# Optimization experiments

Hardware: AMD Instinct MI355X
Metric: run time of the kernel (lower is better)

Reference implementation:

```python
import jax, jax.numpy as jnp
import numpy as np
from jax import lax


def _box_conv3d(x, win):
    k = jnp.ones((1, 1, win, win, win), x.dtype) / float(win ** 3)
    pad = win // 2
    return lax.conv_general_dilated(
        x, k,
        window_strides=(1, 1, 1),
        padding=[(pad, pad)] * 3,
        dimension_numbers=('NCDHW', 'OIDHW', 'NCDHW'),
    )


def setup_inputs() -> dict:
    key = jax.random.key(0)
    k1, k2 = jax.random.split(key)
    shape = (1, 1, 160, 192, 224)
    pred = jax.random.uniform(k1, shape, dtype=jnp.float32)
    target = jax.random.uniform(k2, shape, dtype=jnp.float32)
    return {'pred': pred, 'target': target, 'window_size': 9}


def reference(pred, target, window_size):
    Ii = target
    Ji = pred
    win = window_size
    mu1 = _box_conv3d(Ii, win)
    mu2 = _box_conv3d(Ji, win)
    mu1_sq = mu1 * mu1
    mu2_sq = mu2 * mu2
    mu1_mu2 = mu1 * mu2
    sigma1_sq = _box_conv3d(Ii * Ii, win) - mu1_sq
    sigma2_sq = _box_conv3d(Ji * Ji, win) - mu2_sq
    sigma12 = _box_conv3d(Ii * Ji, win) - mu1_mu2
    eps = jnp.finfo(sigma12.dtype).eps
    cc = sigma12 * sigma12 / jnp.maximum(sigma1_sq * sigma2_sq, eps)
    return -jnp.mean(cc)
```

## Files before the change

### kernel.cpp

```cpp
#include <hip/hip_runtime.h>
#include <hip/hip_fp16.h>

#define D_  160
#define H_  192
#define W_  224
#define HW_ (H_ * W_)
#define HW2_ (HW_ / 2)
#define N_  (D_ * H_ * W_)
#define INV729 (1.0f / 729.0f)
#define HSEG 12
#define NSEG (H_ / HSEG)
#define NROW (HSEG + 9)
#define UPD  (NSEG * 2)


__device__ __forceinline__ unsigned pack2(float a, float b) {
    const __half2 h = __floats2half2_rn(a, b);
    return *(const unsigned*)&h;
}

__global__ __launch_bounds__(256) void k_passWH(const float* __restrict__ pred,
                                                const float* __restrict__ targ,
                                                uint4* __restrict__ outA,
                                                unsigned* __restrict__ outB,
                                                double* __restrict__ acc) {
    __shared__ __attribute__((aligned(16))) float lds[4][2][2][128];
    if (blockIdx.x == 0 && threadIdx.x == 0) *acc = 0.0;

    const int wid  = threadIdx.x >> 6;
    const int lane = threadIdx.x & 63;
    const int unit = blockIdx.x * 4 + wid;
    const int d    = unit / UPD;
    const int rem  = unit % UPD;
    const int half = rem & 1;
    const int h0   = (rem >> 1) * HSEG;
    const long dbase = (long)d * HW_;
    const int wbase = half * 112;

    const bool isld = (lane < 60);
    const int  arr  = (lane >= 30) ? 1 : 0;
    const int  jj   = arr ? lane - 30 : lane;
    const int  ws   = wbase - 4 + 4 * jj;
    const bool geom = isld && (ws >= 0) && (ws + 3 < W_);
    const int  wsc  = ws < 0 ? 0 : (ws > W_ - 4 ? W_ - 4 : ws);
    const float* gsrc = (arr ? pred : targ) + dbase + wsc;

    float2 q[5][9];
    #pragma unroll
    for (int c = 0; c < 5; ++c)
        #pragma unroll
        for (int k = 0; k < 9; ++k) q[c][k] = make_float2(0.f, 0.f);
    float S0[5] = {0,0,0,0,0}, S1[5] = {0,0,0,0,0};

    auto fetch = [&](int p) -> float4 {
        const int hh = h0 - 5 + p;
        const int hc = hh < 0 ? 0 : (hh >= H_ ? H_ - 1 : hh);
        float4 f = *(const float4*)(gsrc + (long)hc * W_);
        if (!(geom && hh >= 0 && hh < H_)) f = make_float4(0.f, 0.f, 0.f, 0.f);
        return f;
    };

    float4 pf[4];
    pf[0] = fetch(0); pf[1] = fetch(1); pf[2] = fetch(2); pf[3] = fetch(3);
    if (isld) *(float4*)&lds[wid][0][arr][4 * jj] = pf[0];
    pf[0] = fetch(4);

    #pragma unroll
    for (int p = 0; p < NROW; ++p) {
        if (isld) *(float4*)&lds[wid][(p + 1) & 1][arr][4 * jj] = pf[(p + 1) & 3];
        pf[(p + 1) & 3] = fetch(p + 5);

        if (lane < 56) {
            float a[10], b[10];
            #pragma unroll
            for (int m = 0; m < 5; ++m) {
                const float2 va = *(const float2*)&lds[wid][p & 1][0][2 * lane + 2 * m];
                const float2 vb = *(const float2*)&lds[wid][p & 1][1][2 * lane + 2 * m];
                a[2*m] = va.x; a[2*m+1] = va.y;
                b[2*m] = vb.x; b[2*m+1] = vb.y;
            }
            float sI = 0.f, sJ = 0.f, sII = 0.f, sJJ = 0.f, sIJ = 0.f;
            #pragma unroll
            for (int kk = 0; kk < 9; ++kk) {
                sI  += a[kk];          sJ  += b[kk];
                sII += a[kk] * a[kk];  sJJ += b[kk] * b[kk];
                sIJ += a[kk] * b[kk];
            }
            float w0[5], w1[5];
            w0[0] = sI;  w1[0] = sI  + a[9] - a[0];
            w0[1] = sJ;  w1[1] = sJ  + b[9] - b[0];
            w0[2] = sII; w1[2] = sII + a[9]*a[9] - a[0]*a[0];
            w0[3] = sJJ; w1[3] = sJJ + b[9]*b[9] - b[0]*b[0];
            w0[4] = sIJ; w1[4] = sIJ + a[9]*b[9] - a[0]*b[0];

            const int ph = p % 9;
            #pragma unroll
            for (int c = 0; c < 5; ++c) {
                S0[c] += w0[c] - q[c][ph].x;
                S1[c] += w1[c] - q[c][ph].y;
                q[c][ph].x = w0[c];
                q[c][ph].y = w1[c];
            }
            if (p >= 9) {
                const long rb = dbase + (long)(h0 + p - 9) * W_;
                uint4 oA;
                oA.x = pack2(S0[0], S0[1]); oA.y = pack2(S0[2], S0[3]);
                oA.z = pack2(S1[0], S1[1]); oA.w = pack2(S1[2], S1[3]);
                outA[rb / 2 + half * 56 + lane] = oA;
                outB[rb / 2 + half * 56 + lane] = pack2(S0[4], S1[4]);
            }
        }
    }
}

__global__ __launch_bounds__(256) void k_passD(const uint4* __restrict__ bufA,
                                               const unsigned* __restrict__ bufB,
                                               double* __restrict__ acc) {
    const int DSEG = D_ / 8;
    const int p2 = blockIdx.x * blockDim.x + threadIdx.x;
    const int d0 = blockIdx.y * DSEG;

    float2 q[5][9], S[5];
    #pragma unroll
    for (int c = 0; c < 5; ++c) S[c] = make_float2(0.f, 0.f);

    #pragma unroll
    for (int k = 0; k < 9; ++k) {
        const int dd = d0 - 5 + k;
        uint4 va = make_uint4(0u, 0u, 0u, 0u);
        unsigned vb = 0u;
        if (dd >= 0) {
            va = bufA[(long)dd * HW2_ + p2];
            vb = bufB[(long)dd * HW2_ + p2];
        }
        const float2 a01 = __half22float2(*(const __half2*)&va.x);
        const float2 a23 = __half22float2(*(const __half2*)&va.y);
        const float2 b01 = __half22float2(*(const __half2*)&va.z);
        const float2 b23 = __half22float2(*(const __half2*)&va.w);
        const float2 c44 = __half22float2(*(const __half2*)&vb);
        q[0][k] = make_float2(a01.x, b01.x); S[0].x += a01.x; S[0].y += b01.x;
        q[1][k] = make_float2(a01.y, b01.y); S[1].x += a01.y; S[1].y += b01.y;
        q[2][k] = make_float2(a23.x, b23.x); S[2].x += a23.x; S[2].y += b23.x;
        q[3][k] = make_float2(a23.y, b23.y); S[3].x += a23.y; S[3].y += b23.y;
        q[4][k] = make_float2(c44.x, c44.y); S[4].x += c44.x; S[4].y += c44.y;
    }

    float myacc = 0.f;
    #pragma unroll
    for (int j = 0; j < DSEG; ++j) {
        const int dd = d0 + 4 + j;
        uint4 va = make_uint4(0u, 0u, 0u, 0u);
        unsigned vb = 0u;
        if (dd < D_) {
            va = bufA[(long)dd * HW2_ + p2];
            vb = bufB[(long)dd * HW2_ + p2];
        }
        const float2 a01 = __half22float2(*(const __half2*)&va.x);
        const float2 a23 = __half22float2(*(const __half2*)&va.y);
        const float2 b01 = __half22float2(*(const __half2*)&va.z);
        const float2 b23 = __half22float2(*(const __half2*)&va.w);
        const float2 c44 = __half22float2(*(const __half2*)&vb);
        const float2 nv[5] = {
            make_float2(a01.x, b01.x), make_float2(a01.y, b01.y),
            make_float2(a23.x, b23.x), make_float2(a23.y, b23.y),
            make_float2(c44.x, c44.y)
        };
        const int ph = j % 9;
        #pragma unroll
        for (int c = 0; c < 5; ++c) {
            S[c].x += nv[c].x - q[c][ph].x;
            S[c].y += nv[c].y - q[c][ph].y;
            q[c][ph] = nv[c];
        }
        #pragma unroll
        for (int e = 0; e < 2; ++e) {
            const float mu1 = (e ? S[0].y : S[0].x) * INV729;
            const float mu2 = (e ? S[1].y : S[1].x) * INV729;
            const float s1  = (e ? S[2].y : S[2].x) * INV729 - mu1 * mu1;
            const float s2  = (e ? S[3].y : S[3].x) * INV729 - mu2 * mu2;
            const float s12 = (e ? S[4].y : S[4].x) * INV729 - mu1 * mu2;
            const float den = fmaxf(s1 * s2, 1.1920929e-7f);
            myacc += (s12 * s12) / den;
        }
    }

    __shared__ float red[256];
    red[threadIdx.x] = myacc;
    __syncthreads();
    #pragma unroll
    for (int s = 128; s > 0; s >>= 1) {
        if (threadIdx.x < s) red[threadIdx.x] += red[threadIdx.x + s];
        __syncthreads();
    }
    if (threadIdx.x == 0) atomicAdd(acc, (double)red[0]);
}

__global__ void k_fin(const double* __restrict__ acc, float* __restrict__ out) {
    out[0] = (float)(-(*acc) / (double)N_);
}

extern "C" void kernel_launch(void* const* d_in, const int* in_sizes, int n_in,
                              void* d_out, int out_size, void* d_ws, size_t ws_size,
                              hipStream_t stream) {
    const float* pred = (const float*)d_in[0];
    const float* targ = (const float*)d_in[1];

    uint4*    bufA = (uint4*)d_ws;
    unsigned* bufB = (unsigned*)((char*)d_ws + (size_t)(N_ / 2) * 16);
    double*   acc  = (double*)((char*)d_ws + (size_t)(N_ / 2) * 16 + (size_t)(N_ / 2) * 4);
    float*    out  = (float*)d_out;

    k_passWH<<<D_ * UPD / 4, 256, 0, stream>>>(pred, targ, bufA, bufB, acc);
    dim3 g3(HW2_ / 256, 8);
    k_passD<<<g3, 256, 0, stream>>>(bufA, bufB, acc);
    k_fin<<<1, 1, 0, stream>>>(acc, out);
}
```

Measured before the change: 56.49 us.

## Stream WH-pass rows straight into LDS with async global_load_lds ring buffer

Replaces the register prefetch plus explicit LDS store in the W/H pass with direct global-to-LDS loads into an 8-slot per-wave ring, waiting on hand-tuned vmcnt counts. Out-of-range rows and chunks read from a small zeroed page, so the masking moves off the load path. The aim is to cut VGPR pressure and the LDS write instructions while keeping about six rows in flight. Accumulator zeroing moves into a separate init kernel, which adds one launch. The vmcnt values depend on how many loads the compiler emits and their order, so any change in code generation could break correctness or stall.

Measured after the change: 65.67 us. +16.3%, slower.

```diff
diff --git a/kernel.cpp b/kernel.cpp
--- a/kernel.cpp
+++ b/kernel.cpp
@@ -12,21 +12,38 @@
 #define NSEG (H_ / HSEG)
 #define NROW (HSEG + 9)
 #define UPD  (NSEG * 2)
-
+#define RING 8
+
+
+typedef __attribute__((address_space(1))) const unsigned GU;
+typedef __attribute__((address_space(3))) unsigned LU;
 
 __device__ __forceinline__ unsigned pack2(float a, float b) {
     const __half2 h = __floats2half2_rn(a, b);
     return *(const unsigned*)&h;
+}
+
+__device__ __forceinline__ void vmwait_step(int p) {
+    if (p <= 9)       asm volatile("s_waitcnt vmcnt(2)"  ::: "memory");
+    else if (p == 10) asm volatile("s_waitcnt vmcnt(4)"  ::: "memory");
+    else if (p == 11) asm volatile("s_waitcnt vmcnt(6)"  ::: "memory");
+    else if (p == 12) asm volatile("s_waitcnt vmcnt(8)"  ::: "memory");
+    else if (p == 13) asm volatile("s_waitcnt vmcnt(10)" ::: "memory");
+    else              asm volatile("s_waitcnt vmcnt(12)" ::: "memory");
+    __builtin_amdgcn_sched_barrier(0);
+}
+
+__global__ void k_init(double* acc, float* zpage) {
+    if (threadIdx.x == 0) *acc = 0.0;
+    if (threadIdx.x < 16) zpage[threadIdx.x] = 0.f;
 }
 
 __global__ __launch_bounds__(256) void k_passWH(const float* __restrict__ pred,
                                                 const float* __restrict__ targ,
                                                 uint4* __restrict__ outA,
                                                 unsigned* __restrict__ outB,
-                                                double* __restrict__ acc) {
-    __shared__ __attribute__((aligned(16))) float lds[4][2][2][128];
-    if (blockIdx.x == 0 && threadIdx.x == 0) *acc = 0.0;
-
+                                                const float* __restrict__ zpage) {
+    __shared__ __attribute__((aligned(16))) float lds[4][RING][256];
     const int wid  = threadIdx.x >> 6;
     const int lane = threadIdx.x & 63;
     const int unit = blockIdx.x * 4 + wid;
@@ -37,13 +54,10 @@
     const long dbase = (long)d * HW_;
     const int wbase = half * 112;
 
-    const bool isld = (lane < 60);
-    const int  arr  = (lane >= 30) ? 1 : 0;
-    const int  jj   = arr ? lane - 30 : lane;
-    const int  ws   = wbase - 4 + 4 * jj;
-    const bool geom = isld && (ws >= 0) && (ws + 3 < W_);
-    const int  wsc  = ws < 0 ? 0 : (ws > W_ - 4 ? W_ - 4 : ws);
-    const float* gsrc = (arr ? pred : targ) + dbase + wsc;
+    const int  jj  = (lane < 30) ? lane : lane - 30;
+    const int  ws  = wbase - 4 + 4 * jj;
+    const bool chunk_ok = (lane < 60) && (ws >= 0) && (ws + 3 < W_);
+    const float* csrc = ((lane < 30) ? targ : pred) + dbase + ws;
 
     float2 q[5][9];
     #pragma unroll
@@ -52,30 +66,26 @@
         for (int k = 0; k < 9; ++k) q[c][k] = make_float2(0.f, 0.f);
     float S0[5] = {0,0,0,0,0}, S1[5] = {0,0,0,0,0};
 
-    auto fetch = [&](int p) -> float4 {
-        const int hh = h0 - 5 + p;
-        const int hc = hh < 0 ? 0 : (hh >= H_ ? H_ - 1 : hh);
-        float4 f = *(const float4*)(gsrc + (long)hc * W_);
-        if (!(geom && hh >= 0 && hh < H_)) f = make_float4(0.f, 0.f, 0.f, 0.f);
-        return f;
+    auto issue = [&](int r) {
+        const int hh = h0 - 5 + r;
+        const bool rok = (hh >= 0) && (hh < H_);
+        const float* ga = (chunk_ok && rok) ? (csrc + (long)hh * W_) : zpage;
+        __builtin_amdgcn_global_load_lds((GU*)ga, (LU*)&lds[wid][r & 7][0], 16, 0, 0);
     };
 
-    float4 pf[4];
-    pf[0] = fetch(0); pf[1] = fetch(1); pf[2] = fetch(2); pf[3] = fetch(3);
-    if (isld) *(float4*)&lds[wid][0][arr][4 * jj] = pf[0];
-    pf[0] = fetch(4);
+    issue(0); issue(1); issue(2); issue(3); issue(4); issue(5);
 
     #pragma unroll
     for (int p = 0; p < NROW; ++p) {
-        if (isld) *(float4*)&lds[wid][(p + 1) & 1][arr][4 * jj] = pf[(p + 1) & 3];
-        pf[(p + 1) & 3] = fetch(p + 5);
+        vmwait_step(p);
 
         if (lane < 56) {
+            const float* buf = &lds[wid][p & 7][0];
             float a[10], b[10];
             #pragma unroll
             for (int m = 0; m < 5; ++m) {
-                const float2 va = *(const float2*)&lds[wid][p & 1][0][2 * lane + 2 * m];
-                const float2 vb = *(const float2*)&lds[wid][p & 1][1][2 * lane + 2 * m];
+                const float2 va = *(const float2*)&buf[2 * lane + 2 * m];
+                const float2 vb = *(const float2*)&buf[120 + 2 * lane + 2 * m];
                 a[2*m] = va.x; a[2*m+1] = va.y;
                 b[2*m] = vb.x; b[2*m+1] = vb.y;
             }
@@ -110,6 +120,8 @@
                 outB[rb / 2 + half * 56 + lane] = pack2(S0[4], S1[4]);
             }
         }
+        issue(p + 6);
+        __builtin_amdgcn_sched_barrier(0);
     }
 }
 
@@ -205,12 +217,19 @@
     const float* pred = (const float*)d_in[0];
     const float* targ = (const float*)d_in[1];
 
-    uint4*    bufA = (uint4*)d_ws;
-    unsigned* bufB = (unsigned*)((char*)d_ws + (size_t)(N_ / 2) * 16);
-    double*   acc  = (double*)((char*)d_ws + (size_t)(N_ / 2) * 16 + (size_t)(N_ / 2) * 4);
-    float*    out  = (float*)d_out;
-
-    k_passWH<<<D_ * UPD / 4, 256, 0, stream>>>(pred, targ, bufA, bufB, acc);
+    const size_t offA = 0;
+    const size_t offB = (size_t)(N_ / 2) * 16;
+    const size_t offAcc = offB + (size_t)(N_ / 2) * 4;
+    const size_t offZ = offAcc + 64;
+
+    uint4*    bufA  = (uint4*)((char*)d_ws + offA);
+    unsigned* bufB  = (unsigned*)((char*)d_ws + offB);
+    double*   acc   = (double*)((char*)d_ws + offAcc);
+    float*    zpage = (float*)((char*)d_ws + offZ);
+    float*    out   = (float*)d_out;
+
+    k_init<<<1, 64, 0, stream>>>(acc, zpage);
+    k_passWH<<<D_ * UPD / 4, 256, 0, stream>>>(pred, targ, bufA, bufB, zpage);
     dim3 g3(HW2_ / 256, 8);
     k_passD<<<g3, 256, 0, stream>>>(bufA, bufB, acc);
     k_fin<<<1, 1, 0, stream>>>(acc, out);
```

## Process full-width rows per wave with 4 outputs per lane and fp16 ring

Applied to the files above, without the earlier changes.

Each wavefront now covers a full 224-wide row strip instead of half, with each lane producing four consecutive W-outputs through a sliding running sum instead of two. The H-direction ring buffer is stored as packed half2 values to cut register pressure, and the launch bound asks for 3 blocks per CU. This halves the number of work units, removes the duplicated halo loads between halves, and amortises the 9-tap sum over more outputs. The trade-off is fewer total waves, which lowers parallelism, and the fp16-rounded ring subtraction may add rounding drift to the running sums.

New measurement: 74.31 us. 31.5% more time.

```diff
diff --git a/kernel.cpp b/kernel.cpp
--- a/kernel.cpp
+++ b/kernel.cpp
@@ -11,7 +11,6 @@
 #define HSEG 12
 #define NSEG (H_ / HSEG)
 #define NROW (HSEG + 9)
-#define UPD  (NSEG * 2)
 
 
 __device__ __forceinline__ unsigned pack2(float a, float b) {
@@ -19,95 +18,132 @@
     return *(const unsigned*)&h;
 }
 
-__global__ __launch_bounds__(256) void k_passWH(const float* __restrict__ pred,
-                                                const float* __restrict__ targ,
-                                                uint4* __restrict__ outA,
-                                                unsigned* __restrict__ outB,
-                                                double* __restrict__ acc) {
-    __shared__ __attribute__((aligned(16))) float lds[4][2][2][128];
+__global__ __launch_bounds__(256, 3) void k_passWH(const float* __restrict__ pred,
+                                                   const float* __restrict__ targ,
+                                                   uint4* __restrict__ outA,
+                                                   unsigned* __restrict__ outB,
+                                                   double* __restrict__ acc) {
+    __shared__ __attribute__((aligned(16))) float lds[4][2][2][240];
     if (blockIdx.x == 0 && threadIdx.x == 0) *acc = 0.0;
 
     const int wid  = threadIdx.x >> 6;
     const int lane = threadIdx.x & 63;
     const int unit = blockIdx.x * 4 + wid;
-    const int d    = unit / UPD;
-    const int rem  = unit % UPD;
-    const int half = rem & 1;
-    const int h0   = (rem >> 1) * HSEG;
+    const int d     = unit / NSEG;
+    const int strip = unit % NSEG;
+    const int h0    = strip * HSEG;
     const long dbase = (long)d * HW_;
-    const int wbase = half * 112;
-
-    const bool isld = (lane < 60);
-    const int  arr  = (lane >= 30) ? 1 : 0;
-    const int  jj   = arr ? lane - 30 : lane;
-    const int  ws   = wbase - 4 + 4 * jj;
-    const bool geom = isld && (ws >= 0) && (ws + 3 < W_);
-    const int  wsc  = ws < 0 ? 0 : (ws > W_ - 4 ? W_ - 4 : ws);
-    const float* gsrc = (arr ? pred : targ) + dbase + wsc;
-
-    float2 q[5][9];
+
+    const int  ws  = 4 * lane - 4;
+    const bool cok = (lane < 58) && (ws >= 0) && (ws + 3 < W_);
+    const int  wsc = ws < 0 ? 0 : (ws > W_ - 4 ? W_ - 4 : ws);
+    const float* gI = targ + dbase + wsc;
+    const float* gJ = pred + dbase + wsc;
+
+    uint2 q[5][9];
     #pragma unroll
     for (int c = 0; c < 5; ++c)
         #pragma unroll
-        for (int k = 0; k < 9; ++k) q[c][k] = make_float2(0.f, 0.f);
-    float S0[5] = {0,0,0,0,0}, S1[5] = {0,0,0,0,0};
-
-    auto fetch = [&](int p) -> float4 {
-        const int hh = h0 - 5 + p;
+        for (int k = 0; k < 9; ++k) q[c][k] = make_uint2(0u, 0u);
+    float S[5][4];
+    #pragma unroll
+    for (int c = 0; c < 5; ++c)
+        #pragma unroll
+        for (int j = 0; j < 4; ++j) S[c][j] = 0.f;
+
+    auto fI = [&](int r) -> float4 {
+        const int hh = h0 - 5 + r;
         const int hc = hh < 0 ? 0 : (hh >= H_ ? H_ - 1 : hh);
-        float4 f = *(const float4*)(gsrc + (long)hc * W_);
-        if (!(geom && hh >= 0 && hh < H_)) f = make_float4(0.f, 0.f, 0.f, 0.f);
+        float4 f = *(const float4*)(gI + (long)hc * W_);
+        if (!(cok && hh >= 0 && hh < H_)) f = make_float4(0.f, 0.f, 0.f, 0.f);
         return f;
     };
-
-    float4 pf[4];
-    pf[0] = fetch(0); pf[1] = fetch(1); pf[2] = fetch(2); pf[3] = fetch(3);
-    if (isld) *(float4*)&lds[wid][0][arr][4 * jj] = pf[0];
-    pf[0] = fetch(4);
+    auto fJ = [&](int r) -> float4 {
+        const int hh = h0 - 5 + r;
+        const int hc = hh < 0 ? 0 : (hh >= H_ ? H_ - 1 : hh);
+        float4 f = *(const float4*)(gJ + (long)hc * W_);
+        if (!(cok && hh >= 0 && hh < H_)) f = make_float4(0.f, 0.f, 0.f, 0.f);
+        return f;
+    };
+
+    float4 pI[2], pJ[2];
+    pI[0] = fI(0); pJ[0] = fJ(0);
+    pI[1] = fI(1); pJ[1] = fJ(1);
+    if (lane < 58) {
+        *(float4*)&lds[wid][0][0][4 * lane] = pI[0];
+        *(float4*)&lds[wid][0][1][4 * lane] = pJ[0];
+    }
+    pI[0] = fI(2); pJ[0] = fJ(2);
 
     #pragma unroll
     for (int p = 0; p < NROW; ++p) {
-        if (isld) *(float4*)&lds[wid][(p + 1) & 1][arr][4 * jj] = pf[(p + 1) & 3];
-        pf[(p + 1) & 3] = fetch(p + 5);
+        const int sl = (p + 1) & 1;
+        const int cb = p & 1;
+        if (lane < 58) {
+            *(float4*)&lds[wid][sl][0][4 * lane] = pI[sl];
+            *(float4*)&lds[wid][sl][1][4 * lane] = pJ[sl];
+        }
+        pI[sl] = fI(p + 3); pJ[sl] = fJ(p + 3);
 
         if (lane < 56) {
-            float a[10], b[10];
+            const float* bI = &lds[wid][cb][0][0];
+            const float* bJ = &lds[wid][cb][1][0];
+            float x[12], y[12];
             #pragma unroll
-            for (int m = 0; m < 5; ++m) {
-                const float2 va = *(const float2*)&lds[wid][p & 1][0][2 * lane + 2 * m];
-                const float2 vb = *(const float2*)&lds[wid][p & 1][1][2 * lane + 2 * m];
-                a[2*m] = va.x; a[2*m+1] = va.y;
-                b[2*m] = vb.x; b[2*m+1] = vb.y;
-            }
-            float sI = 0.f, sJ = 0.f, sII = 0.f, sJJ = 0.f, sIJ = 0.f;
+            for (int m = 0; m < 3; ++m) {
+                const float4 vx = *(const float4*)&bI[4 * lane + 4 * m];
+                const float4 vy = *(const float4*)&bJ[4 * lane + 4 * m];
+                x[4*m] = vx.x; x[4*m+1] = vx.y; x[4*m+2] = vx.z; x[4*m+3] = vx.w;
+                y[4*m] = vy.x; y[4*m+1] = vy.y; y[4*m+2] = vy.z; y[4*m+3] = vy.w;
+            }
+            float wI[4], wJ[4], wII[4], wJJ[4], wIJ[4];
+            float aI = 0.f, aJ = 0.f, aII = 0.f, aJJ = 0.f, aIJ = 0.f;
             #pragma unroll
-            for (int kk = 0; kk < 9; ++kk) {
-                sI  += a[kk];          sJ  += b[kk];
-                sII += a[kk] * a[kk];  sJJ += b[kk] * b[kk];
-                sIJ += a[kk] * b[kk];
-            }
-            float w0[5], w1[5];
-            w0[0] = sI;  w1[0] = sI  + a[9] - a[0];
-            w0[1] = sJ;  w1[1] = sJ  + b[9] - b[0];
-            w0[2] = sII; w1[2] = sII + a[9]*a[9] - a[0]*a[0];
-            w0[3] = sJJ; w1[3] = sJJ + b[9]*b[9] - b[0]*b[0];
-            w0[4] = sIJ; w1[4] = sIJ + a[9]*b[9] - a[0]*b[0];
+            for (int k = 0; k < 9; ++k) {
+                aI += x[k]; aJ += y[k];
+                aII = fmaf(x[k], x[k], aII);
+                aJJ = fmaf(y[k], y[k], aJJ);
+                aIJ = fmaf(x[k], y[k], aIJ);
+            }
+            wI[0] = aI; wJ[0] = aJ; wII[0] = aII; wJJ[0] = aJJ; wIJ[0] = aIJ;
+            #pragma unroll
+            for (int j = 1; j < 4; ++j) {
+                aI  += x[8+j] - x[j-1];
+                aJ  += y[8+j] - y[j-1];
+                aII += x[8+j]*x[8+j] - x[j-1]*x[j-1];
+                aJJ += y[8+j]*y[8+j] - y[j-1]*y[j-1];
+                aIJ += x[8+j]*y[8+j] - x[j-1]*y[j-1];
+                wI[j] = aI; wJ[j] = aJ; wII[j] = aII; wJJ[j] = aJJ; wIJ[j] = aIJ;
+            }
 
             const int ph = p % 9;
-            #pragma unroll
-            for (int c = 0; c < 5; ++c) {
-                S0[c] += w0[c] - q[c][ph].x;
-                S1[c] += w1[c] - q[c][ph].y;
-                q[c][ph].x = w0[c];
-                q[c][ph].y = w1[c];
-            }
+            #define RINGUP(c, W0, W1, W2, W3)                                   \
+            {   const unsigned n01 = pack2(W0, W1), n23 = pack2(W2, W3);        \
+                const float2 f01 = __half22float2(*(const __half2*)&n01);       \
+                const float2 f23 = __half22float2(*(const __half2*)&n23);       \
+                const float2 o01 = __half22float2(*(const __half2*)&q[c][ph].x);\
+                const float2 o23 = __half22float2(*(const __half2*)&q[c][ph].y);\
+                S[c][0] += f01.x - o01.x;  S[c][1] += f01.y - o01.y;            \
+                S[c][2] += f23.x - o23.x;  S[c][3] += f23.y - o23.y;            \
+                q[c][ph] = make_uint2(n01, n23); }
+            RINGUP(0, wI[0],  wI[1],  wI[2],  wI[3])
+            RINGUP(1, wJ[0],  wJ[1],  wJ[2],  wJ[3])
+            RINGUP(2, wII[0], wII[1], wII[2], wII[3])
+            RINGUP(3, wJJ[0], wJJ[1], wJJ[2], wJJ[3])
+            RINGUP(4, wIJ[0], wIJ[1], wIJ[2], wIJ[3])
+            #undef RINGUP
+
             if (p >= 9) {
-                const long rb = dbase + (long)(h0 + p - 9) * W_;
-                uint4 oA;
-                oA.x = pack2(S0[0], S0[1]); oA.y = pack2(S0[2], S0[3]);
-                oA.z = pack2(S1[0], S1[1]); oA.w = pack2(S1[2], S1[3]);
-                outA[rb / 2 + half * 56 + lane] = oA;
-                outB[rb / 2 + half * 56 + lane] = pack2(S0[4], S1[4]);
+                const long rb2 = (dbase + (long)(h0 + p - 9) * W_) / 2;
+                uint4 o0, o1;
+                o0.x = pack2(S[0][0], S[1][0]); o0.y = pack2(S[2][0], S[3][0]);
+                o0.z = pack2(S[0][1], S[1][1]); o0.w = pack2(S[2][1], S[3][1]);
+                o1.x = pack2(S[0][2], S[1][2]); o1.y = pack2(S[2][2], S[3][2]);
+                o1.z = pack2(S[0][3], S[1][3]); o1.w = pack2(S[2][3], S[3][3]);
+                outA[rb2 + 2 * lane]     = o0;
+                outA[rb2 + 2 * lane + 1] = o1;
+                *(uint2*)&outB[rb2 + 2 * lane] =
+                    make_uint2(pack2(S[4][0], S[4][1]), pack2(S[4][2], S[4][3]));
             }
         }
     }
@@ -210,7 +246,7 @@
     double*   acc  = (double*)((char*)d_ws + (size_t)(N_ / 2) * 16 + (size_t)(N_ / 2) * 4);
     float*    out  = (float*)d_out;
 
-    k_passWH<<<D_ * UPD / 4, 256, 0, stream>>>(pred, targ, bufA, bufB, acc);
+    k_passWH<<<D_ * NSEG / 4, 256, 0, stream>>>(pred, targ, bufA, bufB, acc);
     dim3 g3(HW2_ / 256, 8);
     k_passD<<<g3, 256, 0, stream>>>(bufA, bufB, acc);
     k_fin<<<1, 1, 0, stream>>>(acc, out);
```

## Use single-wave blocks, interleaved I/J LDS rows, and taller H segments in W/H pass

Applied to the files above, without the earlier changes.

The W/H pass now runs one 64-lane wave per block instead of four waves sharing a block. Each loading lane fetches both target and pred float4s and writes them interleaved into LDS, so the compute lanes read one float4 per tap pair instead of two float2s. The H segment grows from 12 to 16 rows, which cuts the halo rows re-read per segment. The prefetch depth drops to three slots, and the accumulation uses explicit fma. The trade-off is fewer, longer units and a shallower prefetch queue, with more per-lane load work on the 30 loader lanes.

Measured after the change: 58.37 us. +3.3%, slower.

```diff
diff --git a/kernel.cpp b/kernel.cpp
--- a/kernel.cpp
+++ b/kernel.cpp
@@ -8,7 +8,7 @@
 #define HW2_ (HW_ / 2)
 #define N_  (D_ * H_ * W_)
 #define INV729 (1.0f / 729.0f)
-#define HSEG 12
+#define HSEG 16
 #define NSEG (H_ / HSEG)
 #define NROW (HSEG + 9)
 #define UPD  (NSEG * 2)
@@ -19,17 +19,16 @@
     return *(const unsigned*)&h;
 }
 
-__global__ __launch_bounds__(256) void k_passWH(const float* __restrict__ pred,
-                                                const float* __restrict__ targ,
-                                                uint4* __restrict__ outA,
-                                                unsigned* __restrict__ outB,
-                                                double* __restrict__ acc) {
-    __shared__ __attribute__((aligned(16))) float lds[4][2][2][128];
+__global__ __launch_bounds__(64) void k_passWH(const float* __restrict__ pred,
+                                               const float* __restrict__ targ,
+                                               uint4* __restrict__ outA,
+                                               unsigned* __restrict__ outB,
+                                               double* __restrict__ acc) {
+    __shared__ __attribute__((aligned(16))) float2 lds[2][128];
     if (blockIdx.x == 0 && threadIdx.x == 0) *acc = 0.0;
 
-    const int wid  = threadIdx.x >> 6;
-    const int lane = threadIdx.x & 63;
-    const int unit = blockIdx.x * 4 + wid;
+    const int lane = threadIdx.x;
+    const int unit = blockIdx.x;
     const int d    = unit / UPD;
     const int rem  = unit % UPD;
     const int half = rem & 1;
@@ -37,13 +36,12 @@
     const long dbase = (long)d * HW_;
     const int wbase = half * 112;
 
-    const bool isld = (lane < 60);
-    const int  arr  = (lane >= 30) ? 1 : 0;
-    const int  jj   = arr ? lane - 30 : lane;
-    const int  ws   = wbase - 4 + 4 * jj;
-    const bool geom = isld && (ws >= 0) && (ws + 3 < W_);
-    const int  wsc  = ws < 0 ? 0 : (ws > W_ - 4 ? W_ - 4 : ws);
-    const float* gsrc = (arr ? pred : targ) + dbase + wsc;
+    const bool isld = (lane < 30);
+    const int  w0c  = wbase - 4 + 4 * lane;
+    const bool cok  = isld && (w0c >= 0) && (w0c + 3 < W_);
+    const int  wsc  = w0c < 0 ? 0 : (w0c > W_ - 4 ? W_ - 4 : w0c);
+    const float* gI = targ + dbase + wsc;
+    const float* gJ = pred + dbase + wsc;
 
     float2 q[5][9];
     #pragma unroll
@@ -52,46 +50,60 @@
         for (int k = 0; k < 9; ++k) q[c][k] = make_float2(0.f, 0.f);
     float S0[5] = {0,0,0,0,0}, S1[5] = {0,0,0,0,0};
 
-    auto fetch = [&](int p) -> float4 {
-        const int hh = h0 - 5 + p;
+    float4 pI[3], pJ[3];
+    auto fetch = [&](int r, float4& fi, float4& fj) {
+        if (r >= NROW) { fi = make_float4(0.f,0.f,0.f,0.f); fj = fi; return; }
+        const int hh = h0 - 5 + r;
         const int hc = hh < 0 ? 0 : (hh >= H_ ? H_ - 1 : hh);
-        float4 f = *(const float4*)(gsrc + (long)hc * W_);
-        if (!(geom && hh >= 0 && hh < H_)) f = make_float4(0.f, 0.f, 0.f, 0.f);
-        return f;
+        float4 a = *(const float4*)(gI + (long)hc * W_);
+        float4 b = *(const float4*)(gJ + (long)hc * W_);
+        if (!(cok && hh >= 0 && hh < H_)) {
+            a = make_float4(0.f, 0.f, 0.f, 0.f); b = a;
+        }
+        fi = a; fj = b;
     };
-
-    float4 pf[4];
-    pf[0] = fetch(0); pf[1] = fetch(1); pf[2] = fetch(2); pf[3] = fetch(3);
-    if (isld) *(float4*)&lds[wid][0][arr][4 * jj] = pf[0];
-    pf[0] = fetch(4);
+    auto wr = [&](int row, int slot) {
+        float2* dst = &lds[row & 1][4 * lane];
+        *(float4*)(dst)     = make_float4(pI[slot].x, pJ[slot].x, pI[slot].y, pJ[slot].y);
+        *(float4*)(dst + 2) = make_float4(pI[slot].z, pJ[slot].z, pI[slot].w, pJ[slot].w);
+    };
+
+    if (isld) {
+        fetch(0, pI[0], pJ[0]);
+        fetch(1, pI[1], pJ[1]);
+        fetch(2, pI[2], pJ[2]);
+        wr(0, 0);
+        fetch(3, pI[0], pJ[0]);
+    }
 
     #pragma unroll
     for (int p = 0; p < NROW; ++p) {
-        if (isld) *(float4*)&lds[wid][(p + 1) & 1][arr][4 * jj] = pf[(p + 1) & 3];
-        pf[(p + 1) & 3] = fetch(p + 5);
+        if (isld) {
+            wr(p + 1, (p + 1) % 3);
+            fetch(p + 4, pI[(p + 1) % 3], pJ[(p + 1) % 3]);
+        }
 
         if (lane < 56) {
-            float a[10], b[10];
+            float x[10], y[10];
             #pragma unroll
             for (int m = 0; m < 5; ++m) {
-                const float2 va = *(const float2*)&lds[wid][p & 1][0][2 * lane + 2 * m];
-                const float2 vb = *(const float2*)&lds[wid][p & 1][1][2 * lane + 2 * m];
-                a[2*m] = va.x; a[2*m+1] = va.y;
-                b[2*m] = vb.x; b[2*m+1] = vb.y;
+                const float4 v = *(const float4*)&lds[p & 1][2 * lane + 2 * m];
+                x[2*m] = v.x; y[2*m] = v.y; x[2*m+1] = v.z; y[2*m+1] = v.w;
             }
             float sI = 0.f, sJ = 0.f, sII = 0.f, sJJ = 0.f, sIJ = 0.f;
             #pragma unroll
             for (int kk = 0; kk < 9; ++kk) {
-                sI  += a[kk];          sJ  += b[kk];
-                sII += a[kk] * a[kk];  sJJ += b[kk] * b[kk];
-                sIJ += a[kk] * b[kk];
+                sI  += x[kk];          sJ  += y[kk];
+                sII = fmaf(x[kk], x[kk], sII);
+                sJJ = fmaf(y[kk], y[kk], sJJ);
+                sIJ = fmaf(x[kk], y[kk], sIJ);
             }
             float w0[5], w1[5];
-            w0[0] = sI;  w1[0] = sI  + a[9] - a[0];
-            w0[1] = sJ;  w1[1] = sJ  + b[9] - b[0];
-            w0[2] = sII; w1[2] = sII + a[9]*a[9] - a[0]*a[0];
-            w0[3] = sJJ; w1[3] = sJJ + b[9]*b[9] - b[0]*b[0];
-            w0[4] = sIJ; w1[4] = sIJ + a[9]*b[9] - a[0]*b[0];
+            w0[0] = sI;  w1[0] = sI  + x[9] - x[0];
+            w0[1] = sJ;  w1[1] = sJ  + y[9] - y[0];
+            w0[2] = sII; w1[2] = sII + x[9]*x[9] - x[0]*x[0];
+            w0[3] = sJJ; w1[3] = sJJ + y[9]*y[9] - y[0]*y[0];
+            w0[4] = sIJ; w1[4] = sIJ + x[9]*y[9] - x[0]*y[0];
 
             const int ph = p % 9;
             #pragma unroll
@@ -210,7 +222,7 @@
     double*   acc  = (double*)((char*)d_ws + (size_t)(N_ / 2) * 16 + (size_t)(N_ / 2) * 4);
     float*    out  = (float*)d_out;
 
-    k_passWH<<<D_ * UPD / 4, 256, 0, stream>>>(pred, targ, bufA, bufB, acc);
+    k_passWH<<<D_ * UPD, 64, 0, stream>>>(pred, targ, bufA, bufB, acc);
     dim3 g3(HW2_ / 256, 8);
     k_passD<<<g3, 256, 0, stream>>>(bufA, bufB, acc);
     k_fin<<<1, 1, 0, stream>>>(acc, out);
```
